# Optimization experiments

Hardware: AMD Instinct MI355X
Metric: run time of the kernel (lower is better)

## Reference

```python
import jax, jax.numpy as jnp
import numpy as np

N_NODES = 100000
N_EDGES = 3200000
N_GRAPHS = 1024
F_IN = 4
H = 16


def setup_inputs() -> dict:
    key = jax.random.key(0)
    ks = jax.random.split(key, 12)
    x = jax.random.normal(ks[0], (N_NODES, F_IN), dtype=jnp.float32)
    edge_index = jax.random.randint(ks[1], (2, N_EDGES), 0, N_NODES, dtype=jnp.int64)
    y = jax.random.normal(ks[2], (N_GRAPHS, F_IN), dtype=jnp.float32)
    batch = jnp.sort(jax.random.randint(ks[3], (N_NODES,), 0, N_GRAPHS, dtype=jnp.int64))

    def lin(k, fi, fo):
        s = 1.0 / np.sqrt(fi)
        kw, kb = jax.random.split(k)
        W = jax.random.uniform(kw, (fi, fo), jnp.float32, -s, s)
        b = jax.random.uniform(kb, (fo,), jnp.float32, -s, s)
        return W, b

    W1, b1 = lin(ks[4], F_IN, H)
    W2, b2 = lin(ks[5], H, H)
    W3, b3 = lin(ks[6], H, H)
    fcW1, fcb1 = lin(ks[7], H + 4, H)
    fcW2, fcb2 = lin(ks[8], H, H)
    fcW3, fcb3 = lin(ks[9], H, 1)
    return dict(x=x, edge_index=edge_index, y=y, batch=batch,
                W1=W1, b1=b1, W2=W2, b2=b2, W3=W3, b3=b3,
                fcW1=fcW1, fcb1=fcb1, fcW2=fcW2, fcb2=fcb2, fcW3=fcW3, fcb3=fcb3)


def _gcn_norm(edge_index, n):
    # add self-loops, symmetric normalization (PyG GCNConv default)
    loop = jnp.arange(n, dtype=edge_index.dtype)
    src = jnp.concatenate([edge_index[0], loop])
    dst = jnp.concatenate([edge_index[1], loop])
    deg = jax.ops.segment_sum(jnp.ones_like(dst, dtype=jnp.float32), dst, num_segments=n)
    dinv = jnp.where(deg > 0, jax.lax.rsqrt(deg), 0.0)
    norm = dinv[src] * dinv[dst]  # [E + N]
    return src, dst, norm


def _gcn_conv(x, W, b, src, dst, norm, n):
    h = x @ W                       # [N, out]
    msg = h[src] * norm[:, None]    # gather + scale
    out = jax.ops.segment_sum(msg, dst, num_segments=n)  # scatter-add
    return out + b


def reference(x, edge_index, y, batch, W1, b1, W2, b2, W3, b3,
              fcW1, fcb1, fcW2, fcb2, fcW3, fcb3):
    n = x.shape[0]
    src, dst, norm = _gcn_norm(edge_index, n)
    h = jax.nn.relu(_gcn_conv(x, W1, b1, src, dst, norm, n))
    h = jax.nn.relu(_gcn_conv(h, W2, b2, src, dst, norm, n))
    h = jax.nn.relu(_gcn_conv(h, W3, b3, src, dst, norm, n))
    g = jax.ops.segment_sum(h, batch, num_segments=N_GRAPHS)  # global_add_pool
    g = jnp.concatenate([g, y], axis=1)                       # [G, H+4]
    g = jax.nn.relu(g @ fcW1 + fcb1)
    g = jax.nn.relu(g @ fcW2 + fcb2)
    return g @ fcW3 + fcb3  # [G, 1]
```

## Files before the change

### kernel.cpp

```cpp
#include <hip/hip_runtime.h>
#include <hip/hip_fp16.h>

#define N_NODES 100000
#define N_EDGES 3200000
#define N_GRAPHS 1024
#define F_IN 4
#define H 16

#define NB 256
#define NPB 391
#define CAP 13312
#define CHUNK 4096
#define NBLK ((N_EDGES + CHUNK - 1) / CHUNK)
#define BEPT (CHUNK / 512)
#define EPT_C ((CAP + 1023) / 1024)


__device__ __forceinline__ int lane_id() { return threadIdx.x & 63; }

__device__ __forceinline__ int wave_incl_scan(int v) {
#pragma unroll
    for (int d = 1; d < 64; d <<= 1) {
        int x = __shfl_up(v, d, 64);
        if (lane_id() >= d) v += x;
    }
    return v;
}


__global__ void k_zero_f(float* __restrict__ p, int n) {
    int i = blockIdx.x * blockDim.x + threadIdx.x;
    if (i < n) p[i] = 0.0f;
}


__global__ __launch_bounds__(512) void k_count(const int* __restrict__ dst,
                                               int* __restrict__ blkCnt, int e) {
    __shared__ int h[NB];
    int t = threadIdx.x;
    for (int q = t; q < NB; q += 512) h[q] = 0;
    __syncthreads();
    int e0 = blockIdx.x * CHUNK;
    int e1 = min(e0 + CHUNK, e);
    for (int i = e0 + t; i < e1; i += 512)
        atomicAdd(&h[dst[i] / NPB], 1);
    __syncthreads();
    for (int q = t; q < NB; q += 512) blkCnt[blockIdx.x * NB + q] = h[q];
}

__global__ __launch_bounds__(1024) void k_colscan(const int* __restrict__ blkCnt,
                                                  int* __restrict__ blkBase,
                                                  int* __restrict__ bucketCnt) {
    __shared__ int ws[16];
    __shared__ int wb[16];
    int b = blockIdx.x;
    int t = threadIdx.x;
    int v = (t < NBLK) ? blkCnt[t * NB + b] : 0;
    int incl = wave_incl_scan(v);
    if (lane_id() == 63) ws[t >> 6] = incl;
    __syncthreads();
    if (t == 0) {
        int acc = 0;
#pragma unroll
        for (int q = 0; q < 16; ++q) { wb[q] = acc; acc += ws[q]; }
    }
    __syncthreads();
    int excl = incl - v + wb[t >> 6];
    if (t < NBLK) blkBase[t * NB + b] = excl;
    if (t == NBLK - 1) bucketCnt[b] = excl + v;
}

__global__ void k_scan_buckets(const int* __restrict__ bucketCnt,
                               int* __restrict__ bucketBase) {
    __shared__ int ws[4];
    __shared__ int wb[4];
    int t = threadIdx.x;
    int v = bucketCnt[t];
    int incl = wave_incl_scan(v);
    if (lane_id() == 63) ws[t >> 6] = incl;
    __syncthreads();
    if (t == 0) {
        int acc = 0;
#pragma unroll
        for (int q = 0; q < 4; ++q) { wb[q] = acc; acc += ws[q]; }
    }
    __syncthreads();
    bucketBase[t] = incl - v + wb[t >> 6];
}

__global__ __launch_bounds__(512) void k_place(const int* __restrict__ src,
                                               const int* __restrict__ dst,
                                               const int* __restrict__ bucketBase,
                                               const int* __restrict__ blkBase,
                                               int* __restrict__ ebuf, int e) {
    __shared__ int cnt[NB];
    __shared__ int st[NB];
    __shared__ int lbase[NB];
    __shared__ int ws[4];
    __shared__ int wb[4];
    __shared__ int lsort[CHUNK];
    __shared__ unsigned short bof[CHUNK];
    int t = threadIdx.x;
    for (int q = t; q < NB; q += 512) {
        cnt[q] = 0;
        lbase[q] = bucketBase[q] + blkBase[blockIdx.x * NB + q];
    }
    __syncthreads();
    int e0 = blockIdx.x * CHUNK;
    int e1 = min(e0 + CHUNK, e);
    int m = e1 - e0;
    int vq[BEPT], bq[BEPT], rq[BEPT];
#pragma unroll
    for (int q = 0; q < BEPT; ++q) {
        int i = e0 + t + q * 512;
        bq[q] = -1;
        if (i < e) {
            int s = src[i];
            int d = dst[i];
            int b = d / NPB;
            int l = d - b * NPB;
            vq[q] = s | (l << 20);
            bq[q] = b;
            rq[q] = atomicAdd(&cnt[b], 1);
        }
    }
    __syncthreads();
    int v = (t < NB) ? cnt[t] : 0;
    int incl = wave_incl_scan(v);
    if (t < NB && lane_id() == 63) ws[t >> 6] = incl;
    __syncthreads();
    if (t == 0) {
        int acc = 0;
#pragma unroll
        for (int q = 0; q < 4; ++q) { wb[q] = acc; acc += ws[q]; }
    }
    __syncthreads();
    if (t < NB) st[t] = incl - v + wb[t >> 6];
    __syncthreads();
#pragma unroll
    for (int q = 0; q < BEPT; ++q) {
        if (bq[q] >= 0) {
            int pos = st[bq[q]] + rq[q];
            lsort[pos] = vq[q];
            bof[pos] = (unsigned short)bq[q];
        }
    }
    __syncthreads();
    for (int i = t; i < m; i += 512) {
        int b2 = bof[i];
        ebuf[lbase[b2] + i - st[b2]] = lsort[i];
    }
}

__global__ __launch_bounds__(1024) void k_csrify(const int* __restrict__ ebuf,
                                                 const int* __restrict__ bucketBase,
                                                 const int* __restrict__ bucketCnt,
                                                 const float* __restrict__ x,
                                                 int* __restrict__ csr,
                                                 int* __restrict__ cursor,
                                                 float* __restrict__ dinv,
                                                 __half* __restrict__ ts0) {
    __shared__ int cnt[NPB];
    __shared__ int st[NPB];
    __shared__ int cnt2[NPB];
    __shared__ float sdv[NPB];
    __shared__ int ws[8];
    __shared__ int wb[8];
    __shared__ int lcsr[CAP];
    int t = threadIdx.x;
    int b = blockIdx.x;
    int base = bucketBase[b];
    int m = bucketCnt[b];
    int nbase = b * NPB;
    for (int q = t; q < NPB; q += 1024) { cnt[q] = 0; cnt2[q] = 0; }
    __syncthreads();

    bool fast = (m <= CAP);
    int vq[EPT_C], rq[EPT_C];
    if (fast) {
#pragma unroll
        for (int c = 0; c < EPT_C; ++c) {
            int idx = t + c * 1024;
            vq[c] = -1;
            if (idx < m) {
                int v = ebuf[base + idx];
                vq[c] = v;
                rq[c] = atomicAdd(&cnt[v >> 20], 1);
            }
        }
    } else {
        for (int i = t; i < m; i += 1024)
            atomicAdd(&cnt[ebuf[base + i] >> 20], 1);
    }
    __syncthreads();
    int v0 = (t < NPB) ? cnt[t] : 0;
    int incl = wave_incl_scan(v0);
    if (t < 448 && lane_id() == 63) ws[t >> 6] = incl;
    __syncthreads();
    if (t == 0) {
        int acc = 0;
#pragma unroll
        for (int q = 0; q < 7; ++q) { wb[q] = acc; acc += ws[q]; }
    }
    __syncthreads();
    if (t < NPB) {
        int s = incl - v0 + wb[t >> 6];
        st[t] = s;
        int node = nbase + t;
        if (node < N_NODES) {
            float dv = rsqrtf((float)cnt[t] + 1.0f);
            sdv[t] = dv;
            dinv[node] = dv;
            cursor[node] = base + s + cnt[t];
        }
    }
    __syncthreads();
    for (int idx = t; idx < NPB * F_IN; idx += 1024) {
        int q = idx >> 2;
        int node = nbase + q;
        if (node < N_NODES)
            ts0[node * F_IN + (idx & 3)] =
                __float2half(sdv[q] * x[node * F_IN + (idx & 3)]);
    }
    if (fast) {
#pragma unroll
        for (int c = 0; c < EPT_C; ++c) {
            int v = vq[c];
            if (v >= 0) lcsr[st[v >> 20] + rq[c]] = v & 0xFFFFF;
        }
        __syncthreads();
        for (int i = t; i < m; i += 1024) csr[base + i] = lcsr[i];
    } else {
        for (int i = t; i < m; i += 1024) {
            int v = ebuf[base + i];
            int l = v >> 20;
            int r = atomicAdd(&cnt2[l], 1);
            csr[base + st[l] + r] = v & 0xFFFFF;
        }
    }
}

template <int F, int WAYS>
__global__ void k_gather(const __half* __restrict__ ts, const float* __restrict__ dinv,
                         const int* __restrict__ csr, const int* __restrict__ cursor,
                         float* __restrict__ agg, int n) {
    const int FP = F / 2;
    const int L = FP * WAYS;
    int i = blockIdx.x * (256 / L) + threadIdx.x / L;
    int g = threadIdx.x % L;
    int k2 = g % FP;
    int w = g / FP;
    if (i >= n) return;
    int start = (i == 0) ? 0 : cursor[i - 1];
    int end = cursor[i];
    float ax0 = 0.f, ay0 = 0.f, ax1 = 0.f, ay1 = 0.f;
    int j = start + w;
    for (; j + WAYS < end; j += 2 * WAYS) {
        int s0 = csr[j];
        int s1 = csr[j + WAYS];
        float2 f0 = __half22float2(*(const __half2*)&ts[s0 * F + 2 * k2]);
        float2 f1 = __half22float2(*(const __half2*)&ts[s1 * F + 2 * k2]);
        ax0 += f0.x; ay0 += f0.y;
        ax1 += f1.x; ay1 += f1.y;
    }
    for (; j < end; j += WAYS) {
        float2 f = __half22float2(*(const __half2*)&ts[csr[j] * F + 2 * k2]);
        ax0 += f.x; ay0 += f.y;
    }
    float sx = ax0 + ax1;
    float sy = ay0 + ay1;
    if (w == 0) {
        float2 f = __half22float2(*(const __half2*)&ts[i * F + 2 * k2]);
        sx += f.x; sy += f.y;
    }
#pragma unroll
    for (int msk = FP; msk < L; msk <<= 1) {
        sx += __shfl_xor(sx, msk, 64);
        sy += __shfl_xor(sy, msk, 64);
    }
    if (w == 0) {
        float dv = dinv[i];
        *(float2*)&agg[i * F + 2 * k2] = make_float2(dv * sx, dv * sy);
    }
}

union h4u { float2 f2; __half2 h2[2]; };

__global__ void k_gather16(const __half* __restrict__ ts, const float* __restrict__ dinv,
                           const int* __restrict__ csr, const int* __restrict__ cursor,
                           float* __restrict__ agg, int n) {
    int i = blockIdx.x * 8 + threadIdx.x / 32;
    int g = threadIdx.x & 31;
    int k4 = g & 3;
    int w = g >> 2;
    if (i >= n) return;
    int start = (i == 0) ? 0 : cursor[i - 1];
    int end = cursor[i];
    float ax0 = 0.f, ay0 = 0.f, az0 = 0.f, aw0 = 0.f;
    float ax1 = 0.f, ay1 = 0.f, az1 = 0.f, aw1 = 0.f;
    int j = start + w;
    for (; j + 8 < end; j += 16) {
        int s0 = csr[j];
        int s1 = csr[j + 8];
        h4u u0, u1;
        u0.f2 = *(const float2*)&ts[s0 * H + 4 * k4];
        u1.f2 = *(const float2*)&ts[s1 * H + 4 * k4];
        float2 l0 = __half22float2(u0.h2[0]);
        float2 h0 = __half22float2(u0.h2[1]);
        float2 l1 = __half22float2(u1.h2[0]);
        float2 h1 = __half22float2(u1.h2[1]);
        ax0 += l0.x; ay0 += l0.y; az0 += h0.x; aw0 += h0.y;
        ax1 += l1.x; ay1 += l1.y; az1 += h1.x; aw1 += h1.y;
    }
    for (; j < end; j += 8) {
        h4u u;
        u.f2 = *(const float2*)&ts[csr[j] * H + 4 * k4];
        float2 l = __half22float2(u.h2[0]);
        float2 h = __half22float2(u.h2[1]);
        ax0 += l.x; ay0 += l.y; az0 += h.x; aw0 += h.y;
    }
    float sx = ax0 + ax1, sy = ay0 + ay1, sz = az0 + az1, sw = aw0 + aw1;
    if (w == 0) {
        h4u u;
        u.f2 = *(const float2*)&ts[i * H + 4 * k4];
        float2 l = __half22float2(u.h2[0]);
        float2 h = __half22float2(u.h2[1]);
        sx += l.x; sy += l.y; sz += h.x; sw += h.y;
    }
#pragma unroll
    for (int msk = 4; msk < 32; msk <<= 1) {
        sx += __shfl_xor(sx, msk, 64);
        sy += __shfl_xor(sy, msk, 64);
        sz += __shfl_xor(sz, msk, 64);
        sw += __shfl_xor(sw, msk, 64);
    }
    if (w == 0) {
        float dv = dinv[i];
        *(float4*)&agg[i * H + 4 * k4] = make_float4(dv * sx, dv * sy, dv * sz, dv * sw);
    }
}

template <int FI, bool POOL>
__global__ void k_transform(const float* __restrict__ agg, const float* __restrict__ W,
                            const float* __restrict__ bias, const float* __restrict__ dinv,
                            __half* __restrict__ ts_out, const int* __restrict__ batch,
                            float* __restrict__ g, int n) {
    __shared__ float sW[FI * H];
    for (int t = threadIdx.x; t < FI * H; t += blockDim.x) sW[t] = W[t];
    __syncthreads();
    int i = blockIdx.x * 16 + (threadIdx.x >> 4);
    int k = threadIdx.x & 15;
    if (i >= n) return;
    float acc = bias[k];
#pragma unroll
    for (int j = 0; j < FI; j++) acc = fmaf(agg[i * FI + j], sW[j * H + k], acc);
    float h = fmaxf(acc, 0.0f);
    if (POOL) {
        atomicAdd(&g[batch[i] * H + k], h);
    } else {
        ts_out[i * H + k] = __float2half(dinv[i] * h);
    }
}


__global__ void k_mlp(const float* __restrict__ g, const float* __restrict__ y,
                      const float* __restrict__ fcW1, const float* __restrict__ fcb1,
                      const float* __restrict__ fcW2, const float* __restrict__ fcb2,
                      const float* __restrict__ fcW3, const float* __restrict__ fcb3,
                      float* __restrict__ out, int ngraph) {
    int i = blockIdx.x * blockDim.x + threadIdx.x;
    if (i >= ngraph) return;
    float in[H + 4];
#pragma unroll
    for (int k = 0; k < H; k++) in[k] = g[i * H + k];
#pragma unroll
    for (int k = 0; k < 4; k++) in[H + k] = y[i * 4 + k];
    float z1[H];
#pragma unroll
    for (int o = 0; o < H; o++) {
        float a = fcb1[o];
#pragma unroll
        for (int j = 0; j < H + 4; j++) a += in[j] * fcW1[j * H + o];
        z1[o] = fmaxf(a, 0.0f);
    }
    float z2[H];
#pragma unroll
    for (int o = 0; o < H; o++) {
        float a = fcb2[o];
#pragma unroll
        for (int j = 0; j < H; j++) a += z1[j] * fcW2[j * H + o];
        z2[o] = fmaxf(a, 0.0f);
    }
    float a = fcb3[0];
#pragma unroll
    for (int j = 0; j < H; j++) a += z2[j] * fcW3[j];
    out[i] = a;
}


extern "C" void kernel_launch(void* const* d_in, const int* in_sizes, int n_in,
                              void* d_out, int out_size, void* d_ws, size_t ws_size,
                              hipStream_t stream) {
    const float* x    = (const float*)d_in[0];
    const int*   ei   = (const int*)d_in[1];
    const float* y    = (const float*)d_in[2];
    const int*   bat  = (const int*)d_in[3];
    const float* W1   = (const float*)d_in[4];
    const float* b1   = (const float*)d_in[5];
    const float* W2   = (const float*)d_in[6];
    const float* b2   = (const float*)d_in[7];
    const float* W3   = (const float*)d_in[8];
    const float* b3   = (const float*)d_in[9];
    const float* fcW1 = (const float*)d_in[10];
    const float* fcb1 = (const float*)d_in[11];
    const float* fcW2 = (const float*)d_in[12];
    const float* fcb2 = (const float*)d_in[13];
    const float* fcW3 = (const float*)d_in[14];
    const float* fcb3 = (const float*)d_in[15];
    float* out = (float*)d_out;

    const int* src = ei;
    const int* dst = ei + N_EDGES;

    const int B = 256;
    const int GH = N_GRAPHS * H;
    const int gNode16 = (N_NODES + 15) / 16;
    const int gG4  = (N_NODES + 15) / 16;
    const int gG16 = (N_NODES + 7) / 8;

    char* w = (char*)d_ws;
    size_t off = 0;
    int*    bucketCnt    = (int*)(w + off);    off += (size_t)NB * 4;
    int*    bucketBase   = (int*)(w + off);    off += (size_t)NB * 4;
    int*    blkCnt       = (int*)(w + off);    off += (size_t)NBLK * NB * 4;
    int*    blkBase      = (int*)(w + off);    off += (size_t)NBLK * NB * 4;
    int*    cursor       = (int*)(w + off);    off += (size_t)N_NODES * 4;
    float*  dinv         = (float*)(w + off);  off += (size_t)N_NODES * 4;
    int*    ebuf         = (int*)(w + off);    off += (size_t)N_EDGES * 4;
    int*    csr          = (int*)(w + off);    off += (size_t)N_EDGES * 4;
    __half* ts0          = (__half*)(w + off); off += (size_t)N_NODES * F_IN * 2;
    __half* ts1          = (__half*)(w + off); off += (size_t)N_NODES * H * 2;
    __half* ts2          = (__half*)(w + off); off += (size_t)N_NODES * H * 2;
    float*  agg          = (float*)(w + off);  off += (size_t)N_NODES * H * 4;
    float*  g            = (float*)(w + off);  off += (size_t)GH * 4;
    (void)ws_size;

    k_count<<<NBLK, 512, 0, stream>>>(dst, blkCnt, N_EDGES);
    k_colscan<<<NB, 1024, 0, stream>>>(blkCnt, blkBase, bucketCnt);
    k_scan_buckets<<<1, NB, 0, stream>>>(bucketCnt, bucketBase);
    k_place<<<NBLK, 512, 0, stream>>>(src, dst, bucketBase, blkBase, ebuf, N_EDGES);
    k_csrify<<<NB, 1024, 0, stream>>>(ebuf, bucketBase, bucketCnt, x, csr, cursor,
                                      dinv, ts0);

    k_gather<F_IN, 8><<<gG4, B, 0, stream>>>(ts0, dinv, csr, cursor, agg, N_NODES);
    k_transform<F_IN, false><<<gNode16, B, 0, stream>>>(agg, W1, b1, dinv, ts1,
                                                        nullptr, nullptr, N_NODES);
    k_gather16<<<gG16, B, 0, stream>>>(ts1, dinv, csr, cursor, agg, N_NODES);
    k_transform<H, false><<<gNode16, B, 0, stream>>>(agg, W2, b2, dinv, ts2,
                                                     nullptr, nullptr, N_NODES);
    k_gather16<<<gG16, B, 0, stream>>>(ts2, dinv, csr, cursor, agg, N_NODES);
    k_zero_f<<<(GH + B - 1) / B, B, 0, stream>>>(g, GH);
    k_transform<H, true><<<gNode16, B, 0, stream>>>(agg, W3, b3, dinv, nullptr,
                                                    bat, g, N_NODES);

    k_mlp<<<(N_GRAPHS + B - 1) / B, B, 0, stream>>>(g, y, fcW1, fcb1, fcW2, fcb2,
                                                    fcW3, fcb3, out, N_GRAPHS);
}
```

Measured before the change: 187.7 us.

## Fuse neighbor gather with dense transform per GCN layer via shared memory

```diff
diff --git a/kernel.cpp b/kernel.cpp
--- a/kernel.cpp
+++ b/kernel.cpp
@@ -26,6 +26,9 @@
     }
     return v;
 }
+
+union h4u { float2 f2; __half2 h2[2]; };
+union h8u { float4 f4; __half2 h2[4]; };
 
 
 __global__ void k_zero_f(float* __restrict__ p, int n) {
@@ -240,125 +243,161 @@
     }
 }
 
-template <int F, int WAYS>
-__global__ void k_gather(const __half* __restrict__ ts, const float* __restrict__ dinv,
-                         const int* __restrict__ csr, const int* __restrict__ cursor,
-                         float* __restrict__ agg, int n) {
-    const int FP = F / 2;
-    const int L = FP * WAYS;
-    int i = blockIdx.x * (256 / L) + threadIdx.x / L;
-    int g = threadIdx.x % L;
-    int k2 = g % FP;
-    int w = g / FP;
-    if (i >= n) return;
-    int start = (i == 0) ? 0 : cursor[i - 1];
-    int end = cursor[i];
-    float ax0 = 0.f, ay0 = 0.f, ax1 = 0.f, ay1 = 0.f;
-    int j = start + w;
-    for (; j + WAYS < end; j += 2 * WAYS) {
-        int s0 = csr[j];
-        int s1 = csr[j + WAYS];
-        float2 f0 = __half22float2(*(const __half2*)&ts[s0 * F + 2 * k2]);
-        float2 f1 = __half22float2(*(const __half2*)&ts[s1 * F + 2 * k2]);
-        ax0 += f0.x; ay0 += f0.y;
-        ax1 += f1.x; ay1 += f1.y;
-    }
-    for (; j < end; j += WAYS) {
-        float2 f = __half22float2(*(const __half2*)&ts[csr[j] * F + 2 * k2]);
-        ax0 += f.x; ay0 += f.y;
-    }
-    float sx = ax0 + ax1;
-    float sy = ay0 + ay1;
-    if (w == 0) {
-        float2 f = __half22float2(*(const __half2*)&ts[i * F + 2 * k2]);
-        sx += f.x; sy += f.y;
-    }
-#pragma unroll
-    for (int msk = FP; msk < L; msk <<= 1) {
-        sx += __shfl_xor(sx, msk, 64);
-        sy += __shfl_xor(sy, msk, 64);
-    }
-    if (w == 0) {
-        float dv = dinv[i];
-        *(float2*)&agg[i * F + 2 * k2] = make_float2(dv * sx, dv * sy);
-    }
-}
-
-union h4u { float2 f2; __half2 h2[2]; };
-
-__global__ void k_gather16(const __half* __restrict__ ts, const float* __restrict__ dinv,
-                           const int* __restrict__ csr, const int* __restrict__ cursor,
-                           float* __restrict__ agg, int n) {
-    int i = blockIdx.x * 8 + threadIdx.x / 32;
-    int g = threadIdx.x & 31;
-    int k4 = g & 3;
-    int w = g >> 2;
-    if (i >= n) return;
-    int start = (i == 0) ? 0 : cursor[i - 1];
-    int end = cursor[i];
-    float ax0 = 0.f, ay0 = 0.f, az0 = 0.f, aw0 = 0.f;
-    float ax1 = 0.f, ay1 = 0.f, az1 = 0.f, aw1 = 0.f;
-    int j = start + w;
-    for (; j + 8 < end; j += 16) {
-        int s0 = csr[j];
-        int s1 = csr[j + 8];
-        h4u u0, u1;
-        u0.f2 = *(const float2*)&ts[s0 * H + 4 * k4];
-        u1.f2 = *(const float2*)&ts[s1 * H + 4 * k4];
-        float2 l0 = __half22float2(u0.h2[0]);
-        float2 h0 = __half22float2(u0.h2[1]);
-        float2 l1 = __half22float2(u1.h2[0]);
-        float2 h1 = __half22float2(u1.h2[1]);
-        ax0 += l0.x; ay0 += l0.y; az0 += h0.x; aw0 += h0.y;
-        ax1 += l1.x; ay1 += l1.y; az1 += h1.x; aw1 += h1.y;
-    }
-    for (; j < end; j += 8) {
-        h4u u;
-        u.f2 = *(const float2*)&ts[csr[j] * H + 4 * k4];
-        float2 l = __half22float2(u.h2[0]);
-        float2 h = __half22float2(u.h2[1]);
-        ax0 += l.x; ay0 += l.y; az0 += h.x; aw0 += h.y;
-    }
-    float sx = ax0 + ax1, sy = ay0 + ay1, sz = az0 + az1, sw = aw0 + aw1;
-    if (w == 0) {
-        h4u u;
-        u.f2 = *(const float2*)&ts[i * H + 4 * k4];
-        float2 l = __half22float2(u.h2[0]);
-        float2 h = __half22float2(u.h2[1]);
-        sx += l.x; sy += l.y; sz += h.x; sw += h.y;
-    }
-#pragma unroll
-    for (int msk = 4; msk < 32; msk <<= 1) {
-        sx += __shfl_xor(sx, msk, 64);
-        sy += __shfl_xor(sy, msk, 64);
-        sz += __shfl_xor(sz, msk, 64);
-        sw += __shfl_xor(sw, msk, 64);
-    }
-    if (w == 0) {
-        float dv = dinv[i];
-        *(float4*)&agg[i * H + 4 * k4] = make_float4(dv * sx, dv * sy, dv * sz, dv * sw);
-    }
-}
-
-template <int FI, bool POOL>
-__global__ void k_transform(const float* __restrict__ agg, const float* __restrict__ W,
-                            const float* __restrict__ bias, const float* __restrict__ dinv,
-                            __half* __restrict__ ts_out, const int* __restrict__ batch,
-                            float* __restrict__ g, int n) {
-    __shared__ float sW[FI * H];
-    for (int t = threadIdx.x; t < FI * H; t += blockDim.x) sW[t] = W[t];
-    __syncthreads();
-    int i = blockIdx.x * 16 + (threadIdx.x >> 4);
-    int k = threadIdx.x & 15;
-    if (i >= n) return;
-    float acc = bias[k];
-#pragma unroll
-    for (int j = 0; j < FI; j++) acc = fmaf(agg[i * FI + j], sW[j * H + k], acc);
-    float h = fmaxf(acc, 0.0f);
-    if (POOL) {
-        atomicAdd(&g[batch[i] * H + k], h);
-    } else {
-        ts_out[i * H + k] = __float2half(dinv[i] * h);
+__global__ __launch_bounds__(256) void k_fused1(const __half* __restrict__ ts,
+                                                const float* __restrict__ dinv,
+                                                const int* __restrict__ csr,
+                                                const int* __restrict__ cursor,
+                                                const float* __restrict__ W,
+                                                const float* __restrict__ bias,
+                                                __half* __restrict__ ts_out, int n) {
+    __shared__ float sW[F_IN * H];
+    __shared__ float sagg[16][F_IN];
+    __shared__ float sdv[16];
+    int t = threadIdx.x;
+    if (t < F_IN * H) sW[t] = W[t];
+    int i0 = blockIdx.x * 16;
+    int i = i0 + t / 16;
+    int g = t & 15;
+    int k2 = g & 1;
+    int w = g >> 1;
+    if (i < n) {
+        int start = (i == 0) ? 0 : cursor[i - 1];
+        int end = cursor[i];
+        float ax0 = 0.f, ay0 = 0.f, ax1 = 0.f, ay1 = 0.f;
+        int j = start + w;
+        for (; j + 8 < end; j += 16) {
+            int s0 = csr[j];
+            int s1 = csr[j + 8];
+            float2 f0 = __half22float2(*(const __half2*)&ts[s0 * F_IN + 2 * k2]);
+            float2 f1 = __half22float2(*(const __half2*)&ts[s1 * F_IN + 2 * k2]);
+            ax0 += f0.x; ay0 += f0.y;
+            ax1 += f1.x; ay1 += f1.y;
+        }
+        for (; j < end; j += 8) {
+            float2 f = __half22float2(*(const __half2*)&ts[csr[j] * F_IN + 2 * k2]);
+            ax0 += f.x; ay0 += f.y;
+        }
+        float sx = ax0 + ax1;
+        float sy = ay0 + ay1;
+        if (w == 0) {
+            float2 f = __half22float2(*(const __half2*)&ts[i * F_IN + 2 * k2]);
+            sx += f.x; sy += f.y;
+        }
+#pragma unroll
+        for (int msk = 2; msk < 16; msk <<= 1) {
+            sx += __shfl_xor(sx, msk, 64);
+            sy += __shfl_xor(sy, msk, 64);
+        }
+        if (w == 0) {
+            float dv = dinv[i];
+            int nl = t / 16;
+            sagg[nl][2 * k2] = dv * sx;
+            sagg[nl][2 * k2 + 1] = dv * sy;
+            if (k2 == 0) sdv[nl] = dv;
+        }
+    }
+    __syncthreads();
+    int nl = t >> 4;
+    int k = t & 15;
+    int node = i0 + nl;
+    if (node < n) {
+        float acc = bias[k];
+#pragma unroll
+        for (int j = 0; j < F_IN; j++) acc = fmaf(sagg[nl][j], sW[j * H + k], acc);
+        float h = fmaxf(acc, 0.0f);
+        ts_out[node * H + k] = __float2half(sdv[nl] * h);
+    }
+}
+
+template <bool POOL>
+__global__ __launch_bounds__(256) void k_fused16(const __half* __restrict__ ts,
+                                                 const float* __restrict__ dinv,
+                                                 const int* __restrict__ csr,
+                                                 const int* __restrict__ cursor,
+                                                 const float* __restrict__ W,
+                                                 const float* __restrict__ bias,
+                                                 __half* __restrict__ ts_out,
+                                                 const int* __restrict__ batch,
+                                                 float* __restrict__ g, int n) {
+    __shared__ float sW[H * H];
+    __shared__ float sagg[8][H];
+    __shared__ float sdv[8];
+    int t = threadIdx.x;
+    sW[t] = W[t];
+    int i0 = blockIdx.x * 8;
+    int i = i0 + t / 32;
+    int lg = t & 31;
+    int k8 = lg & 1;
+    int w = lg >> 1;
+    if (i < n) {
+        int start = (i == 0) ? 0 : cursor[i - 1];
+        int end = cursor[i];
+        float a[8] = {0.f, 0.f, 0.f, 0.f, 0.f, 0.f, 0.f, 0.f};
+        float b2[8] = {0.f, 0.f, 0.f, 0.f, 0.f, 0.f, 0.f, 0.f};
+        int j = start + w;
+        for (; j + 16 < end; j += 32) {
+            int s0 = csr[j];
+            int s1 = csr[j + 16];
+            h8u u0, u1;
+            u0.f4 = *(const float4*)&ts[s0 * H + 8 * k8];
+            u1.f4 = *(const float4*)&ts[s1 * H + 8 * k8];
+#pragma unroll
+            for (int q = 0; q < 4; ++q) {
+                float2 f0 = __half22float2(u0.h2[q]);
+                float2 f1 = __half22float2(u1.h2[q]);
+                a[2 * q] += f0.x; a[2 * q + 1] += f0.y;
+                b2[2 * q] += f1.x; b2[2 * q + 1] += f1.y;
+            }
+        }
+        for (; j < end; j += 16) {
+            h8u u;
+            u.f4 = *(const float4*)&ts[csr[j] * H + 8 * k8];
+#pragma unroll
+            for (int q = 0; q < 4; ++q) {
+                float2 f = __half22float2(u.h2[q]);
+                a[2 * q] += f.x; a[2 * q + 1] += f.y;
+            }
+        }
+#pragma unroll
+        for (int q = 0; q < 8; ++q) a[q] += b2[q];
+        if (w == 0) {
+            h8u u;
+            u.f4 = *(const float4*)&ts[i * H + 8 * k8];
+#pragma unroll
+            for (int q = 0; q < 4; ++q) {
+                float2 f = __half22float2(u.h2[q]);
+                a[2 * q] += f.x; a[2 * q + 1] += f.y;
+            }
+        }
+#pragma unroll
+        for (int msk = 2; msk < 32; msk <<= 1) {
+#pragma unroll
+            for (int q = 0; q < 8; ++q) a[q] += __shfl_xor(a[q], msk, 64);
+        }
+        if (w == 0) {
+            float dv = dinv[i];
+            int nl = t / 32;
+#pragma unroll
+            for (int q = 0; q < 8; ++q) sagg[nl][8 * k8 + q] = dv * a[q];
+            if (k8 == 0) sdv[nl] = dv;
+        }
+    }
+    __syncthreads();
+    if (t < 128) {
+        int nl = t >> 4;
+        int k = t & 15;
+        int node = i0 + nl;
+        if (node < n) {
+            float acc = bias[k];
+#pragma unroll
+            for (int j = 0; j < H; j++) acc = fmaf(sagg[nl][j], sW[j * H + k], acc);
+            float h = fmaxf(acc, 0.0f);
+            if (POOL) {
+                atomicAdd(&g[batch[node] * H + k], h);
+            } else {
+                ts_out[node * H + k] = __float2half(sdv[nl] * h);
+            }
+        }
     }
 }
 
@@ -424,9 +463,8 @@
 
     const int B = 256;
     const int GH = N_GRAPHS * H;
-    const int gNode16 = (N_NODES + 15) / 16;
-    const int gG4  = (N_NODES + 15) / 16;
-    const int gG16 = (N_NODES + 7) / 8;
+    const int gF1  = (N_NODES + 15) / 16;
+    const int gF16 = (N_NODES + 7) / 8;
 
     char* w = (char*)d_ws;
     size_t off = 0;
@@ -441,7 +479,6 @@
     __half* ts0          = (__half*)(w + off); off += (size_t)N_NODES * F_IN * 2;
     __half* ts1          = (__half*)(w + off); off += (size_t)N_NODES * H * 2;
     __half* ts2          = (__half*)(w + off); off += (size_t)N_NODES * H * 2;
-    float*  agg          = (float*)(w + off);  off += (size_t)N_NODES * H * 4;
     float*  g            = (float*)(w + off);  off += (size_t)GH * 4;
     (void)ws_size;
 
@@ -452,16 +489,12 @@
     k_csrify<<<NB, 1024, 0, stream>>>(ebuf, bucketBase, bucketCnt, x, csr, cursor,
                                       dinv, ts0);
 
-    k_gather<F_IN, 8><<<gG4, B, 0, stream>>>(ts0, dinv, csr, cursor, agg, N_NODES);
-    k_transform<F_IN, false><<<gNode16, B, 0, stream>>>(agg, W1, b1, dinv, ts1,
-                                                        nullptr, nullptr, N_NODES);
-    k_gather16<<<gG16, B, 0, stream>>>(ts1, dinv, csr, cursor, agg, N_NODES);
-    k_transform<H, false><<<gNode16, B, 0, stream>>>(agg, W2, b2, dinv, ts2,
-                                                     nullptr, nullptr, N_NODES);
-    k_gather16<<<gG16, B, 0, stream>>>(ts2, dinv, csr, cursor, agg, N_NODES);
+    k_fused1<<<gF1, B, 0, stream>>>(ts0, dinv, csr, cursor, W1, b1, ts1, N_NODES);
+    k_fused16<false><<<gF16, B, 0, stream>>>(ts1, dinv, csr, cursor, W2, b2, ts2,
+                                             nullptr, nullptr, N_NODES);
     k_zero_f<<<(GH + B - 1) / B, B, 0, stream>>>(g, GH);
-    k_transform<H, true><<<gNode16, B, 0, stream>>>(agg, W3, b3, dinv, nullptr,
-                                                    bat, g, N_NODES);
+    k_fused16<true><<<gF16, B, 0, stream>>>(ts2, dinv, csr, cursor, W3, b3, nullptr,
+                                            bat, g, N_NODES);
 
     k_mlp<<<(N_GRAPHS + B - 1) / B, B, 0, stream>>>(g, y, fcW1, fcb1, fcW2, fcb2,
                                                     fcW3, fcb3, out, N_GRAPHS);
```

After: 185.6 us. Within noise of the previous version (-1.1%).
